# Performance work log

Measured on AMD Instinct MI355X. Metric: run time of the kernel, lower is better.

Reference implementation:

```python
import jax, jax.numpy as jnp
import numpy as np

# dims
B, F, K = 64, 4096, 8
D_IN = D_SLOT = D_KVQ = 192
HID = 768
N_ITERS = 3
EPS = 1e-8
GROUPS = [(0, 1), (1, 7), (7, 8)]  # bg / fg / ag contiguous slot slices
SB_STRENGTH = 1.0
SB_SIGMA = 0.25
GRID = 64  # sqrt(F)


def _layernorm(x, g, b):
    m = jnp.mean(x, axis=-1, keepdims=True)
    v = jnp.mean(jnp.square(x - m), axis=-1, keepdims=True)
    return (x - m) * jax.lax.rsqrt(v + 1e-5) * g + b


def _gru_cell(x, h, Wih, Whh, bih, bhh):
    # torch.nn.GRUCell semantics; gate order r, z, n
    gi = x @ Wih.T + bih
    gh = h @ Whh.T + bhh
    ir, iz, i_n = jnp.split(gi, 3, axis=-1)
    hr, hz, h_n = jnp.split(gh, 3, axis=-1)
    r = jax.nn.sigmoid(ir + hr)
    z = jax.nn.sigmoid(iz + hz)
    n = jnp.tanh(i_n + r * h_n)
    return (1.0 - z) * n + z * h


def _token_coords():
    y = np.linspace(-1.0, 1.0, GRID, dtype=np.float32)
    x = np.linspace(-1.0, 1.0, GRID, dtype=np.float32)
    yy, xx = np.meshgrid(y, x, indexing='ij')
    return jnp.asarray(np.stack((xx, yy), axis=-1).reshape(F, 2))


def setup_inputs() -> dict:
    key = jax.random.key(0)
    ks = jax.random.split(key, 16)
    def n(i, shape, s=0.02):
        return jax.random.normal(ks[i], shape, jnp.float32) * s
    return dict(
        features=jax.random.normal(ks[0], (B, F, D_IN), jnp.float32),
        slots=jax.random.normal(ks[1], (B, K, D_SLOT), jnp.float32),
        Wk=n(2, (D_IN, D_KVQ)), Wv=n(3, (D_IN, D_KVQ)), Wq=n(4, (D_SLOT, D_KVQ)),
        ln_feat_g=jnp.ones(D_IN), ln_feat_b=jnp.zeros(D_IN),
        ln_slot_g=jnp.ones(D_SLOT), ln_slot_b=jnp.zeros(D_SLOT),
        gru_Wih=n(5, (3, 3 * D_SLOT, D_KVQ)), gru_Whh=n(6, (3, 3 * D_SLOT, D_SLOT)),
        gru_bih=n(7, (3, 3 * D_SLOT)), gru_bhh=n(8, (3, 3 * D_SLOT)),
        mlp_ln_g=jnp.ones((3, D_SLOT)), mlp_ln_b=jnp.zeros((3, D_SLOT)),
        mlp_W1=n(9, (3, D_SLOT, HID)), mlp_b1=n(10, (3, HID)),
        mlp_W2=n(11, (3, HID, D_SLOT)), mlp_b2=n(12, (3, D_SLOT)),
    )


def reference(features, slots, Wk, Wv, Wq, ln_feat_g, ln_feat_b, ln_slot_g,
              ln_slot_b, gru_Wih, gru_Whh, gru_bih, gru_bhh, mlp_ln_g,
              mlp_ln_b, mlp_W1, mlp_b1, mlp_W2, mlp_b2):
    coords = _token_coords()  # (F, 2)
    f = _layernorm(features, ln_feat_g, ln_feat_b)
    k = f @ Wk  # (B, F, Dk)
    v = f @ Wv
    scale = D_KVQ ** -0.5
    sigma2 = max(SB_SIGMA ** 2, 1e-8)
    prev_attn = None
    for _ in range(N_ITERS):
        slots_prev = slots
        q = _layernorm(slots, ln_slot_g, ln_slot_b) @ Wq  # (B, K, Dk)
        dots = jnp.einsum('bkd,bfd->bkf', q, k) * scale
        if prev_attn is not None and SB_STRENGTH > 0.0:
            w = prev_attn / (prev_attn.sum(-1, keepdims=True) + 1e-8)
            centers = jnp.einsum('bkf,fd->bkd', w, coords)  # (B, K, 2)
            diff = coords[None, None] - centers[:, :, None]  # (B, K, F, 2)
            dist2 = jnp.sum(diff * diff, axis=-1)
            dots = dots + SB_STRENGTH * (-dist2 / (2.0 * sigma2))
        attn = jax.nn.softmax(dots, axis=1)  # competition over slots
        prev_attn = attn
        w = attn / (attn.sum(-1, keepdims=True) + EPS)  # weighted mean over F
        updates = jnp.einsum('bkf,bfd->bkd', w, v)  # (B, K, Dk)
        outs = []
        for g, (s, e) in enumerate(GROUPS):
            u = updates[:, s:e].reshape(-1, D_KVQ)
            h_prev = slots_prev[:, s:e].reshape(-1, D_SLOT)
            h = _gru_cell(u, h_prev, gru_Wih[g], gru_Whh[g], gru_bih[g], gru_bhh[g])
            x = _layernorm(h, mlp_ln_g[g], mlp_ln_b[g])
            x = jax.nn.relu(x @ mlp_W1[g] + mlp_b1[g]) @ mlp_W2[g] + mlp_b2[g]
            outs.append((h + x).reshape(B, e - s, D_SLOT))
        slots = jnp.concatenate(outs, axis=1)
    return slots
```

## Files before the change

kernel.cpp:

```cpp
#include <hip/hip_runtime.h>

typedef unsigned short u16;
typedef unsigned int u32;

#define BB 64
#define FF 4096
#define DD 192
#define HH 768

typedef __attribute__((ext_vector_type(8))) __bf16 bf16x8;
typedef __attribute__((ext_vector_type(4))) float f32x4;

__device__ __forceinline__ float bf2f(u32 u) {
  union { u32 i; float f; } x; x.i = u << 16; return x.f;
}
__device__ __forceinline__ u16 f2bf(float f) {
  __bf16 h = (__bf16)f;
  return __builtin_bit_cast(u16, h);
}
__device__ __forceinline__ u32 pk2bf(float a, float b) {
  return (u32)f2bf(a) | ((u32)f2bf(b) << 16);
}
__device__ __forceinline__ float sigm(float x) { return 1.f / (1.f + __expf(-x)); }

__global__ void prep_vw(const float* __restrict__ Wk, const float* __restrict__ Wv,
                        const float* __restrict__ g, const float* __restrict__ bb,
                        float* __restrict__ Wvm, float* __restrict__ s0v,
                        float* __restrict__ s0k) {
  int d = threadIdx.x;
  float av = 0.f, ak = 0.f;
  for (int e = 0; e < DD; ++e) {
    float wv = Wv[e * DD + d];
    Wvm[e * DD + d] = g[e] * wv;
    av += bb[e] * wv;
    ak += bb[e] * Wk[e * DD + d];
  }
  s0v[d] = av; s0k[d] = ak;
}

__global__ void prep_packw(const float* __restrict__ Wih, const float* __restrict__ Whh,
                           const float* __restrict__ W1, const float* __restrict__ W2,
                           u16* __restrict__ pWih, u16* __restrict__ pWhh,
                           u16* __restrict__ pW1, u16* __restrict__ pW2) {
  int which = blockIdx.y;
  int total, N, E;
  const float* src; u16* dst; int srcEmajor;
  if (which < 2) { total = 3 * 576 * 192; N = 576; E = 192; srcEmajor = 0;
                   src = which ? Whh : Wih; dst = which ? pWhh : pWih; }
  else if (which == 2) { total = 3 * 192 * 768; N = 768; E = 192; srcEmajor = 1;
                         src = W1; dst = pW1; }
  else { total = 3 * 768 * 192; N = 192; E = 768; srcEmajor = 1; src = W2; dst = pW2; }
  for (int idx = blockIdx.x * 256 + threadIdx.x; idx < total; idx += gridDim.x * 256) {
    int g = idx / (N * E), rem = idx % (N * E);
    int n, e;
    if (srcEmajor) { e = rem / N; n = rem % N; }
    else { n = rem / E; e = rem % E; }
    dst[((g * (E / 2) + (e >> 1)) * N + n) * 2 + (e & 1)] = f2bf(src[idx]);
  }
}

__global__ __launch_bounds__(256) void fconv(const float* __restrict__ feat,
                                             u16* __restrict__ fb, u16* __restrict__ fd,
                                             float2* __restrict__ stats) {
  __shared__ __align__(16) u16 flds[64 * 192];
  int tid = threadIdx.x;
  int blk = blockIdx.x;
  int r = tid >> 2, p = tid & 3;
  long t = (long)blk * 64 + r;
  const float4* src = (const float4*)(feat + t * DD) + p * 12;
  float s = 0.f, s2 = 0.f;
  long Tg = t >> 4; int tau = (int)(t & 15);
  #pragma unroll
  for (int i = 0; i < 6; ++i) {
    float4 a = src[i * 2], b = src[i * 2 + 1];
    s += a.x + a.y + a.z + a.w + b.x + b.y + b.z + b.w;
    s2 += a.x * a.x + a.y * a.y + a.z * a.z + a.w * a.w +
          b.x * b.x + b.y * b.y + b.z * b.z + b.w * b.w;
    uint4 v;
    v.x = pk2bf(a.x, a.y); v.y = pk2bf(a.z, a.w);
    v.z = pk2bf(b.x, b.y); v.w = pk2bf(b.z, b.w);
    int u = p * 6 + i;
    *(uint4*)(fb + ((Tg * 24 + u) * 16 + tau) * 8) = v;
    *(uint4*)((char*)flds + r * 384 + p * 96 + i * 16) = v;
  }
  s += __shfl_xor(s, 1); s2 += __shfl_xor(s2, 1);
  s += __shfl_xor(s, 2); s2 += __shfl_xor(s2, 2);
  if (p == 0) {
    float mu = s * (1.f / 192.f);
    float rstd = rsqrtf(s2 * (1.f / 192.f) - mu * mu + 1e-5f);
    stats[t] = make_float2(rstd, mu);
  }
  __syncthreads();
  int b = blk >> 6;
  #pragma unroll
  for (int i = 0; i < 6; ++i) {
    int idx = tid + i * 256;
    int tg8 = idx / 192, d = idx % 192;
    u16 h[8];
    #pragma unroll
    for (int j = 0; j < 8; ++j) h[j] = flds[(tg8 * 8 + j) * 192 + d];
    uint4 v;
    v.x = (u32)h[0] | ((u32)h[1] << 16);
    v.y = (u32)h[2] | ((u32)h[3] << 16);
    v.z = (u32)h[4] | ((u32)h[5] << 16);
    v.w = (u32)h[6] | ((u32)h[7] << 16);
    int g32 = (blk & 63) * 2 + (tg8 >> 2);
    int l4f = tg8 & 3;
    *(uint4*)(fd + ((((long)b * 128 + g32) * 12 + (d >> 4)) * 64 + l4f * 16 +
                    (d & 15)) * 8) = v;
  }
}

__global__ __launch_bounds__(64) void qproj_kernel(
    const float* __restrict__ slots, const float* __restrict__ Wq,
    const float* __restrict__ lsg, const float* __restrict__ lsb,
    const float* __restrict__ Wk, const float* __restrict__ lfg,
    const float* __restrict__ s0k,
    u16* __restrict__ pbuf, float* __restrict__ pab,
    float* __restrict__ U, float* __restrict__ scal_cur) {
  __shared__ float ln[192];
  int bk = blockIdx.x;
  int b = bk >> 3, sl = bk & 7;
  int lane = threadIdx.x;
  {
    int gtid = bk * 64 + lane;
    float4 z = {0.f, 0.f, 0.f, 0.f};
    if (gtid < 24576) ((float4*)U)[gtid] = z;
    else if (gtid < 24576 + 512) ((float4*)scal_cur)[gtid - 24576] = z;
  }
  const float* x = slots + bk * DD;
  float v0 = x[lane], v1 = x[lane + 64], v2 = x[lane + 128];
  float s = v0 + v1 + v2, s2 = v0 * v0 + v1 * v1 + v2 * v2;
  #pragma unroll
  for (int m = 1; m < 64; m <<= 1) { s += __shfl_xor(s, m); s2 += __shfl_xor(s2, m); }
  float mu = s * (1.f / 192.f);
  float rstd = rsqrtf(s2 * (1.f / 192.f) - mu * mu + 1e-5f);
  ln[lane]       = (v0 - mu) * rstd * lsg[lane]       + lsb[lane];
  ln[lane + 64]  = (v1 - mu) * rstd * lsg[lane + 64]  + lsb[lane + 64];
  ln[lane + 128] = (v2 - mu) * rstd * lsg[lane + 128] + lsb[lane + 128];
  __syncthreads();
  float a0 = 0.f, a1 = 0.f, a2 = 0.f;
  for (int e = 0; e < DD; ++e) {
    float le = ln[e];
    a0 += le * Wq[e * DD + lane];
    a1 += le * Wq[e * DD + lane + 64];
    a2 += le * Wq[e * DD + lane + 128];
  }
  __syncthreads();
  const float scale = 0.07216878364870323f;
  ln[lane] = a0 * scale; ln[lane + 64] = a1 * scale; ln[lane + 128] = a2 * scale;
  __syncthreads();
  float al = 0.f, be = 0.f;
  u16 pb[3];
  #pragma unroll
  for (int k3 = 0; k3 < 3; ++k3) {
    int d = lane + k3 * 64;
    const float* wr = Wk + (size_t)d * DD;
    float pd = 0.f;
    for (int e = 0; e < DD; ++e) pd += wr[e] * ln[e];
    pd *= lfg[d];
    u16 h = f2bf(pd);
    pb[k3] = h;
    al += bf2f(h);
    be += s0k[d] * ln[d];
  }
  #pragma unroll
  for (int m = 1; m < 64; m <<= 1) { al += __shfl_xor(al, m); be += __shfl_xor(be, m); }
  #pragma unroll
  for (int k3 = 0; k3 < 3; ++k3)
    pbuf[(b * 16 + sl) * DD + lane + k3 * 64] = pb[k3];
  if (lane < 24) *(uint4*)(pbuf + (b * 16 + 8 + sl) * DD + lane * 8) = (uint4){0, 0, 0, 0};
  if (lane == 0) { pab[bk * 2] = al; pab[bk * 2 + 1] = be; }
}

__global__ __launch_bounds__(256) void attnpv_kernel(
    const u16* __restrict__ fb, const u16* __restrict__ fd,
    const u16* __restrict__ pbuf, const float* __restrict__ pab,
    const float2* __restrict__ stats,
    const float* __restrict__ scal_prev,
    float* __restrict__ U, float* __restrict__ scal_cur, int have_bias) {
  __shared__ __align__(16) u16 plds[16 * 192];
  __shared__ __align__(16) u16 attn_lds[16 * 128];
  int b = blockIdx.x;
  int chunk = blockIdx.y * 128;
  int tid = threadIdx.x;
  #pragma unroll
  for (int i = 0; i < 2; ++i) {
    int g = tid + i * 256;
    if (g < 384) {
      int s = g / 24, u = g % 24;
      uint4 v = *(const uint4*)(pbuf + ((b * 16 + s) * DD + u * 8));
      *(uint4*)((char*)plds + s * 384 + ((u ^ (s & 7)) << 4)) = v;
    }
  }
  if (tid < 128) *(uint4*)((char*)attn_lds + 2048 + tid * 16) = (uint4){0, 0, 0, 0};
  __syncthreads();
  int w = tid >> 6, lane = tid & 63;
  int l15 = lane & 15, l4 = lane >> 4;
  bf16x8 qfr[6];
  #pragma unroll
  for (int kk = 0; kk < 6; ++kk) {
    int u = kk * 4 + l4;
    qfr[kk] = *(bf16x8*)((char*)plds + l15 * 384 + ((u ^ (l15 & 7)) << 4));
  }
  float ax[4], ay[4], c0[4], av[4], bv[4];
  #pragma unroll
  for (int j = 0; j < 4; ++j) {
    int s = l4 * 4 + j;
    if (s < 8) {
      av[j] = pab[(b * 8 + s) * 2];
      bv[j] = pab[(b * 8 + s) * 2 + 1];
      if (have_bias) {
        float inv = 1.f / (scal_prev[(b * 8 + s) * 4] + 1e-8f);
        float cx = scal_prev[(b * 8 + s) * 4 + 1] * inv;
        float cy = scal_prev[(b * 8 + s) * 4 + 2] * inv;
        ax[j] = 16.f * cx; ay[j] = 16.f * cy; c0[j] = -8.f * (cx * cx + cy * cy);
      } else { ax[j] = 0.f; ay[j] = 0.f; c0[j] = 0.f; }
    } else { av[j] = 0.f; bv[j] = 0.f; ax[j] = 0.f; ay[j] = 0.f; c0[j] = 0.f; }
  }
  float pa[4], px[4], py[4], pg[4];
  #pragma unroll
  for (int j = 0; j < 4; ++j) { pa[j] = 0.f; px[j] = 0.f; py[j] = 0.f; pg[j] = 0.f; }
  #pragma unroll
  for (int tile = w; tile < 8; tile += 4) {
    int t0 = chunk + tile * 16;
    long Tg = (long)b * 256 + (t0 >> 4);
    const u16* kp = fb + (Tg * 24 + l4) * 128 + l15 * 8;
    f32x4 acc = (f32x4){0.f, 0.f, 0.f, 0.f};
    #pragma unroll
    for (int kk = 0; kk < 6; ++kk) {
      bf16x8 bfr = *(const bf16x8*)(kp + kk * 512);
      acc = __builtin_amdgcn_mfma_f32_16x16x32_bf16(qfr[kk], bfr, acc, 0, 0, 0);
    }
    int t = t0 + l15;
    float2 st = stats[((long)b << 12) + t];
    float rstd = st.x, muv = st.y;
    float x = -1.f + (float)(t & 63) * (2.f / 63.f);
    float y = -1.f + (float)(t >> 6) * (2.f / 63.f);
    float m8r2 = -8.f * (x * x + y * y);
    float d4[4];
    #pragma unroll
    for (int j = 0; j < 4; ++j)
      d4[j] = rstd * acc[j] - rstd * muv * av[j] + bv[j] +
              (have_bias ? (ax[j] * x + ay[j] * y + c0[j] + m8r2) : 0.f);
    float o4[4];
    #pragma unroll
    for (int j = 0; j < 4; ++j) o4[j] = __shfl_xor(d4[j], 16);
    float mx = fmaxf(fmaxf(fmaxf(d4[0], d4[1]), fmaxf(d4[2], d4[3])),
                     fmaxf(fmaxf(o4[0], o4[1]), fmaxf(o4[2], o4[3])));
    float e4[4];
    float sum = 0.f;
    #pragma unroll
    for (int j = 0; j < 4; ++j) { e4[j] = __expf(d4[j] - mx); sum += e4[j]; }
    #pragma unroll
    for (int j = 0; j < 4; ++j) sum += __expf(o4[j] - mx);
    float inv = 1.f / sum;
    if (l4 < 2) {
      int tl = tile * 16 + l15;
      #pragma unroll
      for (int j = 0; j < 4; ++j) {
        float a = e4[j] * inv;
        u16 wr = f2bf(a * rstd);
        int s = l4 * 4 + j;
        *(u16*)((char*)attn_lds + ((s * 256 + tl * 2) ^ ((s & 7) << 4))) = wr;
        pa[j] += a; px[j] += a * x; py[j] += a * y;
        pg[j] += bf2f(wr) * muv;
      }
    }
  }
  #pragma unroll
  for (int m = 1; m < 16; m <<= 1) {
    #pragma unroll
    for (int j = 0; j < 4; ++j) {
      pa[j] += __shfl_xor(pa[j], m);
      px[j] += __shfl_xor(px[j], m);
      py[j] += __shfl_xor(py[j], m);
      pg[j] += __shfl_xor(pg[j], m);
    }
  }
  if (l15 == 0 && l4 < 2) {
    #pragma unroll
    for (int j = 0; j < 4; ++j) {
      int s = l4 * 4 + j;
      atomicAdd(&scal_cur[(b * 8 + s) * 4], pa[j]);
      atomicAdd(&scal_cur[(b * 8 + s) * 4 + 1], px[j]);
      atomicAdd(&scal_cur[(b * 8 + s) * 4 + 2], py[j]);
      atomicAdd(&scal_cur[(b * 8 + s) * 4 + 3], pg[j]);
    }
  }
  __syncthreads();
  int g32base = chunk >> 5;
  #pragma unroll
  for (int ni = 0; ni < 3; ++ni) {
    int nt = w * 3 + ni;
    f32x4 acc = (f32x4){0.f, 0.f, 0.f, 0.f};
    const u16* vp = fd + ((((long)b * 128 + g32base) * 12 + nt) * 64 + l4 * 16 + l15) * 8;
    #pragma unroll
    for (int gl = 0; gl < 4; ++gl) {
      int tl0 = gl * 32 + l4 * 8;
      bf16x8 afr = *(bf16x8*)((char*)attn_lds + ((l15 * 256 + tl0 * 2) ^ ((l15 & 7) << 4)));
      bf16x8 bfr = *(const bf16x8*)(vp + gl * 12 * 64 * 8);
      acc = __builtin_amdgcn_mfma_f32_16x16x32_bf16(afr, bfr, acc, 0, 0, 0);
    }
    if (l4 < 2) {
      #pragma unroll
      for (int j = 0; j < 4; ++j) {
        int s = l4 * 4 + j;
        atomicAdd(&U[((long)b * 8 + s) * DD + nt * 16 + l15], acc[j]);
      }
    }
  }
}

template <int M>
__device__ void gru_body(int b0, int g, int srow,
                         float* u_l, float* h_l, float* gi_l, float* gh_l,
                         float* hn_l, float* ln_l, float* x1_l, float* out_l, float* st,
                         const float* __restrict__ U, const float* __restrict__ scal,
                         const float* __restrict__ Wvm, const float* __restrict__ s0v,
                         const float* __restrict__ sin_,
                         const u16* __restrict__ pWih, const u16* __restrict__ pWhh,
                         const float* __restrict__ bih, const float* __restrict__ bhh,
                         const float* __restrict__ mlng, const float* __restrict__ mlnb,
                         const u16* __restrict__ pW1, const float* __restrict__ b1,
                         const u16* __restrict__ pW2, const float* __restrict__ b2,
                         float* __restrict__ sout) {
  int tid = threadIdx.x;
  for (int idx = tid; idx < M * 192; idx += 768) {
    int row = idx / 192, d = idx % 192;
    int gr = b0 * 8 + srow + row;
    hn_l[row * 192 + d] = U[(long)gr * DD + d];
    h_l[row * 192 + d] = sin_[gr * DD + d];
  }
  __syncthreads();
  if (tid < M * 192) {
    int row = tid / 192, d = tid % 192;
    int gr = b0 * 8 + srow + row;
    float asum = scal[gr * 4], gam = scal[gr * 4 + 3];
    float inv = 1.f / (asum + 1e-8f);
    float acc = asum * s0v[d];
    const float* ur = hn_l + row * 192;
    #pragma unroll 4
    for (int e = 0; e < DD; ++e) acc += (ur[e] - gam) * Wvm[e * DD + d];
    u_l[row * 192 + d] = acc * inv;
  }
  __syncthreads();
  if (tid < 576) {
    int c = tid;
    const u16* wih = pWih + (size_t)g * 96 * 1152 + c * 2;
    const u16* whh = pWhh + (size_t)g * 96 * 1152 + c * 2;
    float ai[M], ah[M];
    #pragma unroll
    for (int r = 0; r < M; ++r) { ai[r] = 0.f; ah[r] = 0.f; }
    #pragma unroll 4
    for (int e2 = 0; e2 < 96; ++e2) {
      u32 wi = *(const u32*)(wih + e2 * 1152);
      u32 wh = *(const u32*)(whh + e2 * 1152);
      float wi0 = bf2f(wi & 0xffffu), wi1 = bf2f(wi >> 16);
      float wh0 = bf2f(wh & 0xffffu), wh1 = bf2f(wh >> 16);
      #pragma unroll
      for (int r = 0; r < M; ++r) {
        ai[r] += wi0 * u_l[r * 192 + e2 * 2] + wi1 * u_l[r * 192 + e2 * 2 + 1];
        ah[r] += wh0 * h_l[r * 192 + e2 * 2] + wh1 * h_l[r * 192 + e2 * 2 + 1];
      }
    }
    #pragma unroll
    for (int r = 0; r < M; ++r) { gi_l[r * 576 + c] = ai[r]; gh_l[r * 576 + c] = ah[r]; }
  }
  __syncthreads();
  if (tid < M * 192) {
    int row = tid / 192, uu = tid % 192;
    const float* bihg = bih + g * 576;
    const float* bhhg = bhh + g * 576;
    float r_ = sigm(gi_l[row * 576 + uu] + bihg[uu] + gh_l[row * 576 + uu] + bhhg[uu]);
    float z_ = sigm(gi_l[row * 576 + 192 + uu] + bihg[192 + uu] +
                    gh_l[row * 576 + 192 + uu] + bhhg[192 + uu]);
    float nn = gi_l[row * 576 + 384 + uu] + bihg[384 + uu] +
               r_ * (gh_l[row * 576 + 384 + uu] + bhhg[384 + uu]);
    float t = 1.f - 2.f / (__expf(2.f * nn) + 1.f);
    hn_l[row * 192 + uu] = (1.f - z_) * t + z_ * h_l[row * 192 + uu];
  }
  __syncthreads();
  {
    int wv = tid >> 6, lane = tid & 63;
    if (wv < M) {
      float v0 = hn_l[wv * 192 + lane], v1 = hn_l[wv * 192 + lane + 64],
            v2 = hn_l[wv * 192 + lane + 128];
      float s = v0 + v1 + v2, sq = v0 * v0 + v1 * v1 + v2 * v2;
      #pragma unroll
      for (int m = 1; m < 64; m <<= 1) { s += __shfl_xor(s, m); sq += __shfl_xor(sq, m); }
      if (lane == 0) {
        float mu = s * (1.f / 192.f);
        st[wv * 2] = mu;
        st[wv * 2 + 1] = rsqrtf(sq * (1.f / 192.f) - mu * mu + 1e-5f);
      }
    }
  }
  __syncthreads();
  if (tid < M * 192) {
    int row = tid / 192, uu = tid % 192;
    ln_l[row * 192 + uu] = (hn_l[row * 192 + uu] - st[row * 2]) * st[row * 2 + 1] *
                               mlng[g * DD + uu] + mlnb[g * DD + uu];
  }
  __syncthreads();
  {
    int c = tid;
    const u16* w1 = pW1 + (size_t)g * 96 * 1536 + c * 2;
    float a[M];
    #pragma unroll
    for (int r = 0; r < M; ++r) a[r] = 0.f;
    #pragma unroll 4
    for (int e2 = 0; e2 < 96; ++e2) {
      u32 wp = *(const u32*)(w1 + e2 * 1536);
      float w0 = bf2f(wp & 0xffffu), w1f = bf2f(wp >> 16);
      #pragma unroll
      for (int r = 0; r < M; ++r)
        a[r] += w0 * ln_l[r * 192 + e2 * 2] + w1f * ln_l[r * 192 + e2 * 2 + 1];
    }
    float bc = b1[g * HH + c];
    #pragma unroll
    for (int r = 0; r < M; ++r) x1_l[r * 768 + c] = fmaxf(a[r] + bc, 0.f);
  }
  if (tid < M * 192) {
    int row = tid / 192, uu = tid % 192;
    out_l[row * 192 + uu] = hn_l[row * 192 + uu] + b2[g * DD + uu];
  }
  __syncthreads();
  {
    int c = tid % 192, ks = tid / 192;
    const u16* w2 = pW2 + (size_t)g * 384 * 384 + c * 2;
    float a[M];
    #pragma unroll
    for (int r = 0; r < M; ++r) a[r] = 0.f;
    #pragma unroll 4
    for (int e2 = ks * 96; e2 < ks * 96 + 96; ++e2) {
      u32 wp = *(const u32*)(w2 + e2 * 384);
      float w0 = bf2f(wp & 0xffffu), w1f = bf2f(wp >> 16);
      #pragma unroll
      for (int r = 0; r < M; ++r)
        a[r] += w0 * x1_l[r * 768 + e2 * 2] + w1f * x1_l[r * 768 + e2 * 2 + 1];
    }
    #pragma unroll
    for (int r = 0; r < M; ++r) atomicAdd(&out_l[r * 192 + c], a[r]);
  }
  __syncthreads();
  if (tid < M * 192) {
    int row = tid / 192, d = tid % 192;
    sout[(b0 * 8 + srow + row) * DD + d] = out_l[row * 192 + d];
  }
}

__global__ __launch_bounds__(768) void gru_kernel(
    const float* __restrict__ U, const float* __restrict__ scal,
    const float* __restrict__ Wvm, const float* __restrict__ s0v,
    const float* __restrict__ sin_,
    const u16* __restrict__ pWih, const u16* __restrict__ pWhh,
    const float* __restrict__ bih, const float* __restrict__ bhh,
    const float* __restrict__ mlng, const float* __restrict__ mlnb,
    const u16* __restrict__ pW1, const float* __restrict__ b1,
    const u16* __restrict__ pW2, const float* __restrict__ b2,
    float* __restrict__ sout) {
  __shared__ float u_l[3 * 192], h_l[3 * 192], gi_l[3 * 576], gh_l[3 * 576];
  __shared__ float hn_l[3 * 192], ln_l[3 * 192], x1_l[3 * 768], out_l[3 * 192], st[8];
  int b = blockIdx.x, y = blockIdx.y;
  if (y == 0)
    gru_body<1>(b, 0, 0, u_l, h_l, gi_l, gh_l, hn_l, ln_l, x1_l, out_l, st,
                U, scal, Wvm, s0v, sin_, pWih, pWhh, bih, bhh, mlng, mlnb,
                pW1, b1, pW2, b2, sout);
  else if (y == 1)
    gru_body<1>(b, 2, 7, u_l, h_l, gi_l, gh_l, hn_l, ln_l, x1_l, out_l, st,
                U, scal, Wvm, s0v, sin_, pWih, pWhh, bih, bhh, mlng, mlnb,
                pW1, b1, pW2, b2, sout);
  else if (y == 2)
    gru_body<3>(b, 1, 1, u_l, h_l, gi_l, gh_l, hn_l, ln_l, x1_l, out_l, st,
                U, scal, Wvm, s0v, sin_, pWih, pWhh, bih, bhh, mlng, mlnb,
                pW1, b1, pW2, b2, sout);
  else
    gru_body<3>(b, 1, 4, u_l, h_l, gi_l, gh_l, hn_l, ln_l, x1_l, out_l, st,
                U, scal, Wvm, s0v, sin_, pWih, pWhh, bih, bhh, mlng, mlnb,
                pW1, b1, pW2, b2, sout);
}

extern "C" void kernel_launch(void* const* d_in, const int* in_sizes, int n_in,
                              void* d_out, int out_size, void* d_ws, size_t ws_size,
                              hipStream_t stream) {
  const float* feat = (const float*)d_in[0];
  const float* slots = (const float*)d_in[1];
  const float* Wk = (const float*)d_in[2];
  const float* Wv = (const float*)d_in[3];
  const float* Wq = (const float*)d_in[4];
  const float* lfg = (const float*)d_in[5];
  const float* lfb = (const float*)d_in[6];
  const float* lsg = (const float*)d_in[7];
  const float* lsb = (const float*)d_in[8];
  const float* gWih = (const float*)d_in[9];
  const float* gWhh = (const float*)d_in[10];
  const float* gbih = (const float*)d_in[11];
  const float* gbhh = (const float*)d_in[12];
  const float* mlng = (const float*)d_in[13];
  const float* mlnb = (const float*)d_in[14];
  const float* W1 = (const float*)d_in[15];
  const float* b1 = (const float*)d_in[16];
  const float* W2 = (const float*)d_in[17];
  const float* b2 = (const float*)d_in[18];
  float* out = (float*)d_out;

  char* ws = (char*)d_ws;
  size_t off = 0;
  auto alloc = [&](size_t bytes) {
    void* p = ws + off;
    off += (bytes + 255) & ~(size_t)255;
    return p;
  };
  u16* fb      = (u16*)alloc((size_t)BB * FF * DD * 2);
  u16* fd      = (u16*)alloc((size_t)BB * DD * FF * 2);
  float2* stats = (float2*)alloc((size_t)BB * FF * 8);
  u16* pbuf    = (u16*)alloc((size_t)BB * 16 * DD * 2);
  float* pab   = (float*)alloc((size_t)BB * 8 * 2 * 4);
  float* U     = (float*)alloc((size_t)BB * 8 * DD * 4);
  float* slA   = (float*)alloc((size_t)BB * 8 * DD * 4);
  float* slB   = (float*)alloc((size_t)BB * 8 * DD * 4);
  float* scal0 = (float*)alloc(BB * 8 * 4 * 4);
  float* scal1 = (float*)alloc(BB * 8 * 4 * 4);
  float* Wvm   = (float*)alloc((size_t)DD * DD * 4);
  float* s0v   = (float*)alloc(DD * 4);
  float* s0k   = (float*)alloc(DD * 4);
  u16* pWih    = (u16*)alloc((size_t)3 * 576 * DD * 2);
  u16* pWhh    = (u16*)alloc((size_t)3 * 576 * DD * 2);
  u16* pW1     = (u16*)alloc((size_t)3 * DD * HH * 2);
  u16* pW2     = (u16*)alloc((size_t)3 * HH * DD * 2);

  prep_vw<<<1, 192, 0, stream>>>(Wk, Wv, lfg, lfb, Wvm, s0v, s0k);
  prep_packw<<<dim3(432, 4), 256, 0, stream>>>(gWih, gWhh, W1, W2, pWih, pWhh, pW1, pW2);
  fconv<<<BB * FF / 64, 256, 0, stream>>>(feat, fb, fd, stats);

  const float* sin_ = slots;
  float* souts[3] = {slA, slB, out};
  float* scals[2] = {scal0, scal1};
  for (int it = 0; it < 3; ++it) {
    int cur = it & 1, prev = cur ^ 1;
    qproj_kernel<<<BB * 8, 64, 0, stream>>>(sin_, Wq, lsg, lsb, Wk, lfg, s0k,
                                            pbuf, pab, U, scals[cur]);
    attnpv_kernel<<<dim3(BB, 32), 256, 0, stream>>>(fb, fd, pbuf, pab, stats,
                                                    scals[prev], U, scals[cur],
                                                    it > 0 ? 1 : 0);
    gru_kernel<<<dim3(BB, 4), 768, 0, stream>>>(U, scals[cur], Wvm, s0v, sin_,
                                                pWih, pWhh, gbih, gbhh, mlng, mlnb,
                                                pW1, b1, pW2, b2, souts[it]);
    sin_ = souts[it];
  }
}
```

Before: 605.0 us.

## Drop transposed feature copy; use LDS transpose reads and partial-sum U buffers

Removes the second, transposed bf16 copy of the features (fd). attnpv now stages each 128-token tile of the single packed copy into LDS through global_load_lds, and reads it both for the QK MFMA and, via ds_read_b64_tr_b16 transpose loads, for the PV MFMA. The float atomicAdd accumulation into U is replaced by per-chunk partial buffers that the GRU kernel sums over 32 chunks, and qproj no longer zeroes U. This cuts global write and read traffic for the features and removes atomics. In exchange it uses about 48KB of LDS per block, which may reduce occupancy, adds an explicit waitcnt inside the PV loop, and adds a 32-way reduction to the GRU kernel.

```diff
diff --git a/kernel.cpp b/kernel.cpp
--- a/kernel.cpp
+++ b/kernel.cpp
@@ -10,6 +10,7 @@
 
 typedef __attribute__((ext_vector_type(8))) __bf16 bf16x8;
 typedef __attribute__((ext_vector_type(4))) float f32x4;
+typedef __attribute__((ext_vector_type(2))) u32 u32x2;
 
 __device__ __forceinline__ float bf2f(u32 u) {
   union { u32 i; float f; } x; x.i = u << 16; return x.f;
@@ -60,16 +61,15 @@
 }
 
 __global__ __launch_bounds__(256) void fconv(const float* __restrict__ feat,
-                                             u16* __restrict__ fb, u16* __restrict__ fd,
+                                             u16* __restrict__ fb,
                                              float2* __restrict__ stats) {
-  __shared__ __align__(16) u16 flds[64 * 192];
+  __shared__ __align__(16) u16 flds[64 * 200];
   int tid = threadIdx.x;
   int blk = blockIdx.x;
   int r = tid >> 2, p = tid & 3;
   long t = (long)blk * 64 + r;
   const float4* src = (const float4*)(feat + t * DD) + p * 12;
   float s = 0.f, s2 = 0.f;
-  long Tg = t >> 4; int tau = (int)(t & 15);
   #pragma unroll
   for (int i = 0; i < 6; ++i) {
     float4 a = src[i * 2], b = src[i * 2 + 1];
@@ -79,9 +79,7 @@
     uint4 v;
     v.x = pk2bf(a.x, a.y); v.y = pk2bf(a.z, a.w);
     v.z = pk2bf(b.x, b.y); v.w = pk2bf(b.z, b.w);
-    int u = p * 6 + i;
-    *(uint4*)(fb + ((Tg * 24 + u) * 16 + tau) * 8) = v;
-    *(uint4*)((char*)flds + r * 384 + p * 96 + i * 16) = v;
+    *(uint4*)((char*)flds + r * 400 + p * 96 + i * 16) = v;
   }
   s += __shfl_xor(s, 1); s2 += __shfl_xor(s2, 1);
   s += __shfl_xor(s, 2); s2 += __shfl_xor(s2, 2);
@@ -91,23 +89,18 @@
     stats[t] = make_float2(rstd, mu);
   }
   __syncthreads();
-  int b = blk >> 6;
+  u16* fbc = fb + (size_t)(blk >> 1) * 24576;
+  int half = blk & 1;
   #pragma unroll
   for (int i = 0; i < 6; ++i) {
-    int idx = tid + i * 256;
-    int tg8 = idx / 192, d = idx % 192;
-    u16 h[8];
-    #pragma unroll
-    for (int j = 0; j < 8; ++j) h[j] = flds[(tg8 * 8 + j) * 192 + d];
-    uint4 v;
-    v.x = (u32)h[0] | ((u32)h[1] << 16);
-    v.y = (u32)h[2] | ((u32)h[3] << 16);
-    v.z = (u32)h[4] | ((u32)h[5] << 16);
-    v.w = (u32)h[6] | ((u32)h[7] << 16);
-    int g32 = (blk & 63) * 2 + (tg8 >> 2);
-    int l4f = tg8 & 3;
-    *(uint4*)(fd + ((((long)b * 128 + g32) * 12 + (d >> 4)) * 64 + l4f * 16 +
-                    (d & 15)) * 8) = v;
+    int q = tid + i * 256;
+    int nt = q / 128, within = q % 128;
+    int T4loc = within >> 3, sub = within & 7;
+    int tloc = T4loc * 4 + (sub >> 1);
+    int d0 = nt * 16 + (sub & 1) * 8;
+    uint4 v = *(uint4*)(flds + tloc * 200 + d0);
+    int slot = nt * 256 + (half * 16 + T4loc) * 8 + sub;
+    *(uint4*)(fbc + slot * 8) = v;
   }
 }
 
@@ -117,16 +110,14 @@
     const float* __restrict__ Wk, const float* __restrict__ lfg,
     const float* __restrict__ s0k,
     u16* __restrict__ pbuf, float* __restrict__ pab,
-    float* __restrict__ U, float* __restrict__ scal_cur) {
+    float* __restrict__ scal_cur) {
   __shared__ float ln[192];
   int bk = blockIdx.x;
   int b = bk >> 3, sl = bk & 7;
   int lane = threadIdx.x;
   {
     int gtid = bk * 64 + lane;
-    float4 z = {0.f, 0.f, 0.f, 0.f};
-    if (gtid < 24576) ((float4*)U)[gtid] = z;
-    else if (gtid < 24576 + 512) ((float4*)scal_cur)[gtid - 24576] = z;
+    if (gtid < 512) ((float4*)scal_cur)[gtid] = (float4){0.f, 0.f, 0.f, 0.f};
   }
   const float* x = slots + bk * DD;
   float v0 = x[lane], v1 = x[lane + 64], v2 = x[lane + 128];
@@ -174,16 +165,17 @@
 }
 
 __global__ __launch_bounds__(256) void attnpv_kernel(
-    const u16* __restrict__ fb, const u16* __restrict__ fd,
-    const u16* __restrict__ pbuf, const float* __restrict__ pab,
-    const float2* __restrict__ stats,
+    const u16* __restrict__ fb, const u16* __restrict__ pbuf,
+    const float* __restrict__ pab, const float2* __restrict__ stats,
     const float* __restrict__ scal_prev,
-    float* __restrict__ U, float* __restrict__ scal_cur, int have_bias) {
+    float* __restrict__ U_part, float* __restrict__ scal_cur, int have_bias) {
+  __shared__ __align__(16) u16 ftile[24576];
   __shared__ __align__(16) u16 plds[16 * 192];
   __shared__ __align__(16) u16 attn_lds[16 * 128];
-  int b = blockIdx.x;
-  int chunk = blockIdx.y * 128;
+  int b = blockIdx.x, cy = blockIdx.y;
   int tid = threadIdx.x;
+  int w = tid >> 6, lane = tid & 63;
+  int l15 = lane & 15, l4 = lane >> 4;
   #pragma unroll
   for (int i = 0; i < 2; ++i) {
     int g = tid + i * 256;
@@ -194,9 +186,16 @@
     }
   }
   if (tid < 128) *(uint4*)((char*)attn_lds + 2048 + tid * 16) = (uint4){0, 0, 0, 0};
-  __syncthreads();
-  int w = tid >> 6, lane = tid & 63;
-  int l15 = lane & 15, l4 = lane >> 4;
+  {
+    const u16* fbc = fb + (size_t)(b * 32 + cy) * 24576;
+    #pragma unroll
+    for (int j = 0; j < 12; ++j) {
+      int g = w * 768 + j * 64;
+      __builtin_amdgcn_global_load_lds((const u32*)(fbc + (size_t)(g + lane) * 8),
+                                       (u32*)&ftile[g * 8], 16, 0, 0);
+    }
+  }
+  __syncthreads();
   bf16x8 qfr[6];
   #pragma unroll
   for (int kk = 0; kk < 6; ++kk) {
@@ -213,8 +212,8 @@
       if (have_bias) {
         float inv = 1.f / (scal_prev[(b * 8 + s) * 4] + 1e-8f);
         float cx = scal_prev[(b * 8 + s) * 4 + 1] * inv;
-        float cy = scal_prev[(b * 8 + s) * 4 + 2] * inv;
-        ax[j] = 16.f * cx; ay[j] = 16.f * cy; c0[j] = -8.f * (cx * cx + cy * cy);
+        float cy2 = scal_prev[(b * 8 + s) * 4 + 2] * inv;
+        ax[j] = 16.f * cx; ay[j] = 16.f * cy2; c0[j] = -8.f * (cx * cx + cy2 * cy2);
       } else { ax[j] = 0.f; ay[j] = 0.f; c0[j] = 0.f; }
     } else { av[j] = 0.f; bv[j] = 0.f; ax[j] = 0.f; ay[j] = 0.f; c0[j] = 0.f; }
   }
@@ -222,17 +221,18 @@
   #pragma unroll
   for (int j = 0; j < 4; ++j) { pa[j] = 0.f; px[j] = 0.f; py[j] = 0.f; pg[j] = 0.f; }
   #pragma unroll
-  for (int tile = w; tile < 8; tile += 4) {
-    int t0 = chunk + tile * 16;
-    long Tg = (long)b * 256 + (t0 >> 4);
-    const u16* kp = fb + (Tg * 24 + l4) * 128 + l15 * 8;
+  for (int tt = 0; tt < 2; ++tt) {
+    int tile = w + tt * 4;
+    int t128 = tile * 16 + l15;
+    int trow = (t128 >> 2) * 64 + (t128 & 3) * 16;
     f32x4 acc = (f32x4){0.f, 0.f, 0.f, 0.f};
     #pragma unroll
     for (int kk = 0; kk < 6; ++kk) {
-      bf16x8 bfr = *(const bf16x8*)(kp + kk * 512);
+      int u = kk * 4 + l4;
+      bf16x8 bfr = *(bf16x8*)(ftile + (u >> 1) * 2048 + trow + (u & 1) * 8);
       acc = __builtin_amdgcn_mfma_f32_16x16x32_bf16(qfr[kk], bfr, acc, 0, 0, 0);
     }
-    int t = t0 + l15;
+    int t = cy * 128 + t128;
     float2 st = stats[((long)b << 12) + t];
     float rstd = st.x, muv = st.y;
     float x = -1.f + (float)(t & 63) * (2.f / 63.f);
@@ -256,13 +256,15 @@
     for (int j = 0; j < 4; ++j) sum += __expf(o4[j] - mx);
     float inv = 1.f / sum;
     if (l4 < 2) {
-      int tl = tile * 16 + l15;
+      int t5 = t128 & 31;
+      int kidx = ((t5 >> 2) & 3) * 8 + ((t5 >> 4) & 1) * 4 + (t5 & 3);
+      int k128 = (t128 & ~31) | kidx;
       #pragma unroll
       for (int j = 0; j < 4; ++j) {
         float a = e4[j] * inv;
         u16 wr = f2bf(a * rstd);
         int s = l4 * 4 + j;
-        *(u16*)((char*)attn_lds + ((s * 256 + tl * 2) ^ ((s & 7) << 4))) = wr;
+        *(u16*)((char*)attn_lds + ((s * 256 + k128 * 2) ^ ((s & 7) << 4))) = wr;
         pa[j] += a; px[j] += a * x; py[j] += a * y;
         pg[j] += bf2f(wr) * muv;
       }
@@ -289,25 +291,37 @@
     }
   }
   __syncthreads();
-  int g32base = chunk >> 5;
+  u32 ldsbase = (u32)(size_t)&ftile[0];
+  f32x4 pacc[3];
+  #pragma unroll
+  for (int ni = 0; ni < 3; ++ni) pacc[ni] = (f32x4){0.f, 0.f, 0.f, 0.f};
   #pragma unroll
   for (int ni = 0; ni < 3; ++ni) {
     int nt = w * 3 + ni;
-    f32x4 acc = (f32x4){0.f, 0.f, 0.f, 0.f};
-    const u16* vp = fd + ((((long)b * 128 + g32base) * 12 + nt) * 64 + l4 * 16 + l15) * 8;
-    #pragma unroll
-    for (int gl = 0; gl < 4; ++gl) {
-      int tl0 = gl * 32 + l4 * 8;
-      bf16x8 afr = *(bf16x8*)((char*)attn_lds + ((l15 * 256 + tl0 * 2) ^ ((l15 & 7) << 4)));
-      bf16x8 bfr = *(const bf16x8*)(vp + gl * 12 * 64 * 8);
-      acc = __builtin_amdgcn_mfma_f32_16x16x32_bf16(afr, bfr, acc, 0, 0, 0);
-    }
-    if (l4 < 2) {
+    #pragma unroll
+    for (int g = 0; g < 4; ++g) {
+      u32 a = ldsbase + nt * 4096 + g * 1024 + lane * 8;
+      u32x2 lo, hi;
+      asm volatile("ds_read_b64_tr_b16 %0, %2\n\t"
+                   "ds_read_b64_tr_b16 %1, %2 offset:512"
+                   : "=&v"(lo), "=&v"(hi) : "v"(a));
+      asm volatile("s_waitcnt lgkmcnt(0)" ::: "memory");
+      __builtin_amdgcn_sched_barrier(0);
+      union { u32 u[4]; bf16x8 v; } bb_;
+      bb_.u[0] = lo.x; bb_.u[1] = lo.y; bb_.u[2] = hi.x; bb_.u[3] = hi.y;
+      bf16x8 afr = *(bf16x8*)((char*)attn_lds +
+                              ((l15 * 256 + g * 64 + l4 * 16) ^ ((l15 & 7) << 4)));
+      pacc[ni] = __builtin_amdgcn_mfma_f32_16x16x32_bf16(afr, bb_.v, pacc[ni], 0, 0, 0);
+    }
+  }
+  if (l4 < 2) {
+    float* up = U_part + (size_t)(b * 32 + cy) * 1536;
+    #pragma unroll
+    for (int ni = 0; ni < 3; ++ni) {
+      int nt = w * 3 + ni;
       #pragma unroll
-      for (int j = 0; j < 4; ++j) {
-        int s = l4 * 4 + j;
-        atomicAdd(&U[((long)b * 8 + s) * DD + nt * 16 + l15], acc[j]);
-      }
+      for (int j = 0; j < 4; ++j)
+        up[(l4 * 4 + j) * 192 + nt * 16 + l15] = pacc[ni][j];
     }
   }
 }
@@ -316,7 +330,7 @@
 __device__ void gru_body(int b0, int g, int srow,
                          float* u_l, float* h_l, float* gi_l, float* gh_l,
                          float* hn_l, float* ln_l, float* x1_l, float* out_l, float* st,
-                         const float* __restrict__ U, const float* __restrict__ scal,
+                         const float* __restrict__ U_part, const float* __restrict__ scal,
                          const float* __restrict__ Wvm, const float* __restrict__ s0v,
                          const float* __restrict__ sin_,
                          const u16* __restrict__ pWih, const u16* __restrict__ pWhh,
@@ -329,7 +343,11 @@
   for (int idx = tid; idx < M * 192; idx += 768) {
     int row = idx / 192, d = idx % 192;
     int gr = b0 * 8 + srow + row;
-    hn_l[row * 192 + d] = U[(long)gr * DD + d];
+    float acc = 0.f;
+    const float* upb = U_part + (size_t)b0 * 32 * 1536 + (srow + row) * 192 + d;
+    #pragma unroll 4
+    for (int c = 0; c < 32; ++c) acc += upb[c * 1536];
+    hn_l[row * 192 + d] = acc;
     h_l[row * 192 + d] = sin_[gr * DD + d];
   }
   __syncthreads();
@@ -451,7 +469,7 @@
 }
 
 __global__ __launch_bounds__(768) void gru_kernel(
-    const float* __restrict__ U, const float* __restrict__ scal,
+    const float* __restrict__ U_part, const float* __restrict__ scal,
     const float* __restrict__ Wvm, const float* __restrict__ s0v,
     const float* __restrict__ sin_,
     const u16* __restrict__ pWih, const u16* __restrict__ pWhh,
@@ -465,19 +483,19 @@
   int b = blockIdx.x, y = blockIdx.y;
   if (y == 0)
     gru_body<1>(b, 0, 0, u_l, h_l, gi_l, gh_l, hn_l, ln_l, x1_l, out_l, st,
-                U, scal, Wvm, s0v, sin_, pWih, pWhh, bih, bhh, mlng, mlnb,
+                U_part, scal, Wvm, s0v, sin_, pWih, pWhh, bih, bhh, mlng, mlnb,
                 pW1, b1, pW2, b2, sout);
   else if (y == 1)
     gru_body<1>(b, 2, 7, u_l, h_l, gi_l, gh_l, hn_l, ln_l, x1_l, out_l, st,
-                U, scal, Wvm, s0v, sin_, pWih, pWhh, bih, bhh, mlng, mlnb,
+                U_part, scal, Wvm, s0v, sin_, pWih, pWhh, bih, bhh, mlng, mlnb,
                 pW1, b1, pW2, b2, sout);
   else if (y == 2)
     gru_body<3>(b, 1, 1, u_l, h_l, gi_l, gh_l, hn_l, ln_l, x1_l, out_l, st,
-                U, scal, Wvm, s0v, sin_, pWih, pWhh, bih, bhh, mlng, mlnb,
+                U_part, scal, Wvm, s0v, sin_, pWih, pWhh, bih, bhh, mlng, mlnb,
                 pW1, b1, pW2, b2, sout);
   else
     gru_body<3>(b, 1, 4, u_l, h_l, gi_l, gh_l, hn_l, ln_l, x1_l, out_l, st,
-                U, scal, Wvm, s0v, sin_, pWih, pWhh, bih, bhh, mlng, mlnb,
+                U_part, scal, Wvm, s0v, sin_, pWih, pWhh, bih, bhh, mlng, mlnb,
                 pW1, b1, pW2, b2, sout);
 }
 
@@ -512,27 +530,26 @@
     off += (bytes + 255) & ~(size_t)255;
     return p;
   };
-  u16* fb      = (u16*)alloc((size_t)BB * FF * DD * 2);
-  u16* fd      = (u16*)alloc((size_t)BB * DD * FF * 2);
+  u16* fb       = (u16*)alloc((size_t)BB * FF * DD * 2);
   float2* stats = (float2*)alloc((size_t)BB * FF * 8);
-  u16* pbuf    = (u16*)alloc((size_t)BB * 16 * DD * 2);
-  float* pab   = (float*)alloc((size_t)BB * 8 * 2 * 4);
-  float* U     = (float*)alloc((size_t)BB * 8 * DD * 4);
-  float* slA   = (float*)alloc((size_t)BB * 8 * DD * 4);
-  float* slB   = (float*)alloc((size_t)BB * 8 * DD * 4);
-  float* scal0 = (float*)alloc(BB * 8 * 4 * 4);
-  float* scal1 = (float*)alloc(BB * 8 * 4 * 4);
-  float* Wvm   = (float*)alloc((size_t)DD * DD * 4);
-  float* s0v   = (float*)alloc(DD * 4);
-  float* s0k   = (float*)alloc(DD * 4);
-  u16* pWih    = (u16*)alloc((size_t)3 * 576 * DD * 2);
-  u16* pWhh    = (u16*)alloc((size_t)3 * 576 * DD * 2);
-  u16* pW1     = (u16*)alloc((size_t)3 * DD * HH * 2);
-  u16* pW2     = (u16*)alloc((size_t)3 * HH * DD * 2);
+  u16* pbuf     = (u16*)alloc((size_t)BB * 16 * DD * 2);
+  float* pab    = (float*)alloc((size_t)BB * 8 * 2 * 4);
+  float* U_part = (float*)alloc((size_t)BB * 32 * 8 * DD * 4);
+  float* slA    = (float*)alloc((size_t)BB * 8 * DD * 4);
+  float* slB    = (float*)alloc((size_t)BB * 8 * DD * 4);
+  float* scal0  = (float*)alloc(BB * 8 * 4 * 4);
+  float* scal1  = (float*)alloc(BB * 8 * 4 * 4);
+  float* Wvm    = (float*)alloc((size_t)DD * DD * 4);
+  float* s0v    = (float*)alloc(DD * 4);
+  float* s0k    = (float*)alloc(DD * 4);
+  u16* pWih     = (u16*)alloc((size_t)3 * 576 * DD * 2);
+  u16* pWhh     = (u16*)alloc((size_t)3 * 576 * DD * 2);
+  u16* pW1      = (u16*)alloc((size_t)3 * DD * HH * 2);
+  u16* pW2      = (u16*)alloc((size_t)3 * HH * DD * 2);
 
   prep_vw<<<1, 192, 0, stream>>>(Wk, Wv, lfg, lfb, Wvm, s0v, s0k);
   prep_packw<<<dim3(432, 4), 256, 0, stream>>>(gWih, gWhh, W1, W2, pWih, pWhh, pW1, pW2);
-  fconv<<<BB * FF / 64, 256, 0, stream>>>(feat, fb, fd, stats);
+  fconv<<<BB * FF / 64, 256, 0, stream>>>(feat, fb, stats);
 
   const float* sin_ = slots;
   float* souts[3] = {slA, slB, out};
@@ -540,11 +557,11 @@
   for (int it = 0; it < 3; ++it) {
     int cur = it & 1, prev = cur ^ 1;
     qproj_kernel<<<BB * 8, 64, 0, stream>>>(sin_, Wq, lsg, lsb, Wk, lfg, s0k,
-                                            pbuf, pab, U, scals[cur]);
-    attnpv_kernel<<<dim3(BB, 32), 256, 0, stream>>>(fb, fd, pbuf, pab, stats,
-                                                    scals[prev], U, scals[cur],
+                                            pbuf, pab, scals[cur]);
+    attnpv_kernel<<<dim3(BB, 32), 256, 0, stream>>>(fb, pbuf, pab, stats,
+                                                    scals[prev], U_part, scals[cur],
                                                     it > 0 ? 1 : 0);
-    gru_kernel<<<dim3(BB, 4), 768, 0, stream>>>(U, scals[cur], Wvm, s0v, sin_,
+    gru_kernel<<<dim3(BB, 4), 768, 0, stream>>>(U_part, scals[cur], Wvm, s0v, sin_,
                                                 pWih, pWhh, gbih, gbhh, mlng, mlnb,
                                                 pW1, b1, pW2, b2, souts[it]);
     sin_ = souts[it];
```

Measured after the change: 536.7 us. -11.3%, faster.
